# Kernel optimization log

Measured on AMD Instinct MI355X. Metric: run time of the kernel, lower is better.

## Reference

```python
import jax, jax.numpy as jnp
import numpy as np

N_EXPERTS = 16
NUM_SHARDS = 1
CAPACITY_FACTOR = 1.25
EPS = 0.01


def setup_inputs() -> dict:
    key = jax.random.key(0)
    k1, k2, k3 = jax.random.split(key, 3)
    C, T, D = 4, 4096, 1024
    E = N_EXPERTS * NUM_SHARDS
    inputs = jax.random.normal(k1, (C, T, D), dtype=jnp.float32)
    # trunc-normal router weight, std = (initializer_factor / ((D + E)/2))**0.5
    std = (1.0 / ((D + E) / 2.0)) ** 0.5
    router_weight = jax.random.truncated_normal(k2, -2.0, 2.0, (E, D), dtype=jnp.float32) * std
    # multiplicative jitter in [1-eps, 1+eps)
    noise = (1.0 - EPS) + 2.0 * EPS * jax.random.uniform(k3, (C, T, D), dtype=jnp.float32)
    return {"inputs": inputs, "router_weight": router_weight, "noise": noise}


def reference(inputs, router_weight, noise):
    C, T, D = inputs.shape
    E = N_EXPERTS * NUM_SHARDS
    expert_capacity = max(int(CAPACITY_FACTOR * T // N_EXPERTS), 1)

    x = inputs.astype(jnp.float32) * noise                      # gate inputs with jitter
    router_logits = jnp.einsum('ctd,ed->cte', x, router_weight)  # [C,T,E]
    router_probs = jax.nn.softmax(router_logits, axis=-1)
    expert_gate = jnp.max(router_probs, axis=-1)                 # [C,T]
    expert_index = jnp.argmax(router_probs, axis=-1)             # [C,T] int

    expert_mask = jax.nn.one_hot(expert_index, E, dtype=jnp.float32)  # [C,T,E]

    # load-balancing aux loss (before capacity truncation)
    density1 = expert_mask.mean(axis=1)          # [C,E]
    density1_proxy = router_probs.mean(axis=1)   # [C,E]
    aux_loss = (density1 * density1_proxy).sum() * E

    # capacity-limited position tracking
    position_in_expert = jnp.cumsum(expert_mask, axis=1) * expert_mask            # [C,T,E]
    expert_mask = expert_mask * (position_in_expert.astype(jnp.int32) < expert_capacity)
    expert_mask_flat = expert_mask.sum(axis=-1)                                    # [C,T]
    position_in_expert = (jnp.cumsum(expert_mask, axis=1) * expert_mask).astype(jnp.int32)
    expert_gate = expert_gate * expert_mask_flat

    # Faithful replication of torch scatter_(dim=1) on a [C,T,E,1] tensor with
    # index shape [C,T,1,1]: only the (e=0, cap=0) slice is written, at token
    # position == expert_index[c,t].
    c_idx = jnp.arange(C)[:, None]
    expert_index_inf = jnp.zeros((C, T, E, 1), jnp.float32).at[c_idx, expert_index, 0, 0].set(1.0)

    # one-hot over capacity slot (scatter along dim 3)
    position_inf = jax.nn.one_hot(position_in_expert, expert_capacity, dtype=jnp.float32)  # [C,T,E,cap]

    combine_tensor = (expert_gate[:, :, None, None]
                      * expert_mask_flat[:, :, None, None]
                      * expert_index_inf
                      * position_inf)
    dispatch_tensor = combine_tensor.astype(bool)
    return dispatch_tensor, combine_tensor, aux_loss
```

## Files before the change

kernel.cpp:

```cpp
#include <hip/hip_runtime.h>
#include <math.h>

#define C_DIM 4
#define T_DIM 4096
#define D_DIM 1024
#define E_DIM 16
#define CAP   320
#define CT    (C_DIM * T_DIM)
#define OUT_ONE ((size_t)CT * E_DIM * CAP)

#define NBLOCKS 2048
#define N4      ((2 * OUT_ONE) / 4)
#define F4_PER_BLOCK (N4 / NBLOCKS)

__host__ __device__ constexpr int bitrev5(int i) {
    return ((i & 1) << 4) | ((i & 2) << 2) | (i & 4) | ((i & 8) >> 2) | ((i & 16) >> 4);
}


__device__ __forceinline__ void do_router(
    const float* __restrict__ in, const float* __restrict__ w,
    const float* __restrict__ noise, float* __restrict__ gate,
    int* __restrict__ index, float* psum, int* hcnt)
{
    const int tid  = threadIdx.x;
    const int wave = tid >> 6;
    const int lane = tid & 63;
    const int g0   = blockIdx.x * 8 + wave * 2;

    float val[32];
    #pragma unroll
    for (int i = 0; i < 32; ++i) val[i] = 0.0f;

    #pragma unroll
    for (int r = 0; r < 4; ++r) {
        const int d0 = r * 256 + lane * 4;
        float4 x[2];
        #pragma unroll
        for (int tk = 0; tk < 2; ++tk) {
            const float4 a = *(const float4*)(in    + (size_t)(g0 + tk) * D_DIM + d0);
            const float4 n = *(const float4*)(noise + (size_t)(g0 + tk) * D_DIM + d0);
            x[tk] = make_float4(a.x * n.x, a.y * n.y, a.z * n.z, a.w * n.w);
        }
        #pragma unroll
        for (int e = 0; e < 16; ++e) {
            const float4 wv = *(const float4*)(w + e * D_DIM + d0);
            #pragma unroll
            for (int tk = 0; tk < 2; ++tk) {
                val[bitrev5(tk * 16 + e)] += x[tk].x * wv.x + x[tk].y * wv.y
                                           + x[tk].z * wv.z + x[tk].w * wv.w;
            }
        }
    }

    #pragma unroll
    for (int m = 0; m < 5; ++m) {
        const int half = 16 >> m;
        const int bit  = (lane >> m) & 1;
        #pragma unroll
        for (int j = 0; j < half; ++j) {
            const float send = bit ? val[j] : val[j + half];
            const float recv = __shfl_xor(send, 1 << m, 64);
            val[j] = (bit ? val[j + half] : val[j]) + recv;
        }
    }
    float logit = val[0];
    logit += __shfl_xor(logit, 32, 64);

    const int tk = (lane >> 4) & 1;
    const int e  = lane & 15;
    const int g  = g0 + tk;

    float mv = logit; int am = e;
    #pragma unroll
    for (int msk = 1; msk <= 8; msk <<= 1) {
        const float ov = __shfl_xor(mv, msk, 64);
        const int   oe = __shfl_xor(am, msk, 64);
        if (ov > mv || (ov == mv && oe < am)) { mv = ov; am = oe; }
    }

    const float p = __expf(logit - mv);
    float s = p;
    #pragma unroll
    for (int msk = 1; msk <= 8; msk <<= 1)
        s += __shfl_xor(s, msk, 64);

    const float inv = 1.0f / s;
    if (lane < 32 && e == am) {
        gate[g]  = inv;
        index[g] = am;
        atomicAdd(&hcnt[am], 1);
    }

    float pn = p * inv;
    pn += __shfl_xor(pn, 16, 64);
    if (lane < 16)
        atomicAdd(&psum[e], pn);
}

__device__ __forceinline__ void do_fill(float4* __restrict__ out4)
{
    const float4 z = make_float4(0.f, 0.f, 0.f, 0.f);
    float4* dst = out4 + (size_t)blockIdx.x * F4_PER_BLOCK;
    #pragma unroll 8
    for (int i = threadIdx.x; i < F4_PER_BLOCK; i += 256)
        dst[i] = z;
}

__global__ __launch_bounds__(256) void fused_router_fill_kernel(
    const float* __restrict__ in, const float* __restrict__ w,
    const float* __restrict__ noise, float* __restrict__ gate,
    int* __restrict__ index, float* __restrict__ auxpart,
    int* __restrict__ counts, float4* __restrict__ out4)
{
    __shared__ float psum[E_DIM];
    __shared__ int   hcnt[E_DIM];
    const int tid = threadIdx.x;
    if (tid < E_DIM) { psum[tid] = 0.0f; hcnt[tid] = 0; }
    __syncthreads();

    if (blockIdx.x & 1) {
        do_fill(out4);
        do_router(in, w, noise, gate, index, psum, hcnt);
    } else {
        do_router(in, w, noise, gate, index, psum, hcnt);
        do_fill(out4);
    }

    __syncthreads();
    if (tid < 16) {
        const int c = blockIdx.x >> 9;
        atomicAdd(&auxpart[c * 16 + tid], psum[tid]);
        atomicAdd(&counts [c * 16 + tid], hcnt[tid]);
    }
}

__global__ __launch_bounds__(64) void finalize_kernel(
    const float* __restrict__ gate, const int* __restrict__ index,
    const int* __restrict__ counts, const float* __restrict__ auxpart,
    float* __restrict__ out)
{
    const int id = threadIdx.x;
    const int c  = id >> 4;
    const int tp = id & 15;
    const int cnt = counts[id];

    float term = ((float)cnt * (1.0f / T_DIM)) * (auxpart[id] * (1.0f / T_DIM));

    if (cnt > 0) {
        const int g     = c * T_DIM + tp;
        const int myidx = index[g];
        int s = 0;
        if (myidx == 0) {
            int r = 0;
            for (int t = 0; t <= tp; ++t)
                r += (index[c * T_DIM + t] == 0);
            s = r;
        }
        const size_t off = ((size_t)g * E_DIM + 0) * CAP + (size_t)s;
        out[off]            = 1.0f;
        out[OUT_ONE + off]  = gate[g];
    }

    #pragma unroll
    for (int off = 32; off; off >>= 1)
        term += __shfl_down(term, off, 64);
    if (id == 0)
        out[2 * OUT_ONE] = 16.0f * term;
}

extern "C" void kernel_launch(void* const* d_in, const int* in_sizes, int n_in,
                              void* d_out, int out_size, void* d_ws, size_t ws_size,
                              hipStream_t stream) {
    const float* in    = (const float*)d_in[0];
    const float* w     = (const float*)d_in[1];
    const float* noise = (const float*)d_in[2];
    float* out = (float*)d_out;

    char* ws = (char*)d_ws;
    float* auxpart = (float*)(ws);
    int*   counts  = (int*)(ws + 256);
    float* gate    = (float*)(ws + 512);
    int*   index   = (int*)(ws + 512 + 65536);

    (void)hipMemsetAsync(ws, 0, 512, stream);

    fused_router_fill_kernel<<<dim3(NBLOCKS), dim3(256), 0, stream>>>(
        in, w, noise, gate, index, auxpart, counts, (float4*)out);
    finalize_kernel<<<dim3(1), dim3(64), 0, stream>>>(gate, index, counts, auxpart, out);
}
```

Before: 179.1 us.

## Double-buffer router input loads via global_load_lds asynchronous staging

The router's input and noise loads now go through per-wave LDS double buffers filled with global_load_lds. Manual s_waitcnt counters let the next chunk load while the current one is computed. The intent is to hide global load latency behind the dot products. The kernel now uses 32KB of LDS per block, which may lower occupancy, and the handwritten waitcnt values depend on the order the compiler emits instructions in.

```diff
diff --git a/kernel.cpp b/kernel.cpp
--- a/kernel.cpp
+++ b/kernel.cpp
@@ -18,40 +18,96 @@
 }
 
 
-__device__ __forceinline__ void do_router(
+__device__ __forceinline__ void gl_lds16(const float* g, float* l) {
+    __builtin_amdgcn_global_load_lds(
+        (const __attribute__((address_space(1))) void*)g,
+        (__attribute__((address_space(3))) void*)l,
+        16, 0, 0);
+}
+
+__device__ __forceinline__ void stage_chunk(
+    const float* __restrict__ in, const float* __restrict__ noise,
+    float (*buf)[256], int g0, int r, int lane)
+{
+    const size_t base = (size_t)g0 * D_DIM + r * 256 + lane * 4;
+    gl_lds16(in    + base,                  &buf[0][0]);
+    gl_lds16(in    + base + D_DIM,          &buf[1][0]);
+    gl_lds16(noise + base,                  &buf[2][0]);
+    gl_lds16(noise + base + D_DIM,          &buf[3][0]);
+}
+
+__device__ __forceinline__ void compute_chunk(
+    const float* __restrict__ w, float (*buf)[256], float* val, int r, int lane)
+{
+    const int d0 = r * 256 + lane * 4;
+    float4 x[2];
+    #pragma unroll
+    for (int tk = 0; tk < 2; ++tk) {
+        const float4 a = *(const float4*)&buf[tk][lane * 4];
+        const float4 n = *(const float4*)&buf[2 + tk][lane * 4];
+        x[tk] = make_float4(a.x * n.x, a.y * n.y, a.z * n.z, a.w * n.w);
+    }
+    #pragma unroll
+    for (int e = 0; e < 16; ++e) {
+        const float4 wv = *(const float4*)(w + e * D_DIM + d0);
+        #pragma unroll
+        for (int tk = 0; tk < 2; ++tk)
+            val[bitrev5(tk * 16 + e)] += x[tk].x * wv.x + x[tk].y * wv.y
+                                       + x[tk].z * wv.z + x[tk].w * wv.w;
+    }
+}
+
+__global__ __launch_bounds__(256) void fused_router_fill_kernel(
     const float* __restrict__ in, const float* __restrict__ w,
     const float* __restrict__ noise, float* __restrict__ gate,
-    int* __restrict__ index, float* psum, int* hcnt)
-{
-    const int tid  = threadIdx.x;
+    int* __restrict__ index, float* __restrict__ auxpart,
+    int* __restrict__ counts, float4* __restrict__ out4)
+{
+    __shared__ float stage_lds[4][2][4][256];
+    __shared__ float psum[E_DIM];
+    __shared__ int   hcnt[E_DIM];
+    const int tid = threadIdx.x;
+    if (tid < E_DIM) { psum[tid] = 0.0f; hcnt[tid] = 0; }
+    __syncthreads();
+
     const int wave = tid >> 6;
     const int lane = tid & 63;
     const int g0   = blockIdx.x * 8 + wave * 2;
 
+    const float4 z = make_float4(0.f, 0.f, 0.f, 0.f);
+    float4* dst = out4 + (size_t)blockIdx.x * F4_PER_BLOCK;
+
+    if (blockIdx.x & 1) {
+        #pragma unroll 8
+        for (int i = tid; i < F4_PER_BLOCK; i += 256)
+            dst[i] = z;
+    }
+
     float val[32];
     #pragma unroll
     for (int i = 0; i < 32; ++i) val[i] = 0.0f;
 
-    #pragma unroll
-    for (int r = 0; r < 4; ++r) {
-        const int d0 = r * 256 + lane * 4;
-        float4 x[2];
-        #pragma unroll
-        for (int tk = 0; tk < 2; ++tk) {
-            const float4 a = *(const float4*)(in    + (size_t)(g0 + tk) * D_DIM + d0);
-            const float4 n = *(const float4*)(noise + (size_t)(g0 + tk) * D_DIM + d0);
-            x[tk] = make_float4(a.x * n.x, a.y * n.y, a.z * n.z, a.w * n.w);
-        }
-        #pragma unroll
-        for (int e = 0; e < 16; ++e) {
-            const float4 wv = *(const float4*)(w + e * D_DIM + d0);
-            #pragma unroll
-            for (int tk = 0; tk < 2; ++tk) {
-                val[bitrev5(tk * 16 + e)] += x[tk].x * wv.x + x[tk].y * wv.y
-                                           + x[tk].z * wv.z + x[tk].w * wv.w;
-            }
-        }
-    }
+    float (*sbuf0)[256] = stage_lds[wave][0];
+    float (*sbuf1)[256] = stage_lds[wave][1];
+
+    stage_chunk(in, noise, sbuf0, g0, 0, lane);
+    stage_chunk(in, noise, sbuf1, g0, 1, lane);
+
+    asm volatile("s_waitcnt vmcnt(4)" ::: "memory");
+    compute_chunk(w, sbuf0, val, 0, lane);
+    asm volatile("s_waitcnt lgkmcnt(0)" ::: "memory");
+    stage_chunk(in, noise, sbuf0, g0, 2, lane);
+
+    asm volatile("s_waitcnt vmcnt(4)" ::: "memory");
+    compute_chunk(w, sbuf1, val, 1, lane);
+    asm volatile("s_waitcnt lgkmcnt(0)" ::: "memory");
+    stage_chunk(in, noise, sbuf1, g0, 3, lane);
+
+    asm volatile("s_waitcnt vmcnt(4)" ::: "memory");
+    compute_chunk(w, sbuf0, val, 2, lane);
+
+    asm volatile("s_waitcnt vmcnt(0)" ::: "memory");
+    compute_chunk(w, sbuf1, val, 3, lane);
 
     #pragma unroll
     for (int m = 0; m < 5; ++m) {
@@ -96,42 +152,18 @@
     pn += __shfl_xor(pn, 16, 64);
     if (lane < 16)
         atomicAdd(&psum[e], pn);
-}
-
-__device__ __forceinline__ void do_fill(float4* __restrict__ out4)
-{
-    const float4 z = make_float4(0.f, 0.f, 0.f, 0.f);
-    float4* dst = out4 + (size_t)blockIdx.x * F4_PER_BLOCK;
-    #pragma unroll 8
-    for (int i = threadIdx.x; i < F4_PER_BLOCK; i += 256)
-        dst[i] = z;
-}
-
-__global__ __launch_bounds__(256) void fused_router_fill_kernel(
-    const float* __restrict__ in, const float* __restrict__ w,
-    const float* __restrict__ noise, float* __restrict__ gate,
-    int* __restrict__ index, float* __restrict__ auxpart,
-    int* __restrict__ counts, float4* __restrict__ out4)
-{
-    __shared__ float psum[E_DIM];
-    __shared__ int   hcnt[E_DIM];
-    const int tid = threadIdx.x;
-    if (tid < E_DIM) { psum[tid] = 0.0f; hcnt[tid] = 0; }
-    __syncthreads();
-
-    if (blockIdx.x & 1) {
-        do_fill(out4);
-        do_router(in, w, noise, gate, index, psum, hcnt);
-    } else {
-        do_router(in, w, noise, gate, index, psum, hcnt);
-        do_fill(out4);
-    }
 
     __syncthreads();
     if (tid < 16) {
         const int c = blockIdx.x >> 9;
         atomicAdd(&auxpart[c * 16 + tid], psum[tid]);
         atomicAdd(&counts [c * 16 + tid], hcnt[tid]);
+    }
+
+    if (!(blockIdx.x & 1)) {
+        #pragma unroll 8
+        for (int i = tid; i < F4_PER_BLOCK; i += 256)
+            dst[i] = z;
     }
 }
 
```

New measurement: 193.4 us. 8.0% more time.
